# Kernel optimization log

Measured on AMD Instinct MI355X. Metric: run time of the kernel, lower is better.

Reference implementation:

```python
import jax, jax.numpy as jnp
import numpy as np

EMBED_DIM = 1024
NUM_HEADS = 16
HEAD_DIM = EMBED_DIM // NUM_HEADS  # 64
MLP_DIM = 4096
EPS = 1e-5  # torch LayerNorm default


def layer_norm(x, gamma, beta):
    mu = jnp.mean(x, axis=-1, keepdims=True)
    var = jnp.mean(jnp.square(x - mu), axis=-1, keepdims=True)
    return (x - mu) * jax.lax.rsqrt(var + EPS) * gamma + beta


def setup_inputs() -> dict:
    key = jax.random.key(0)
    ks = jax.random.split(key, 12)
    s = 0.02
    x = jax.random.normal(ks[0], (2, 2048, EMBED_DIM), dtype=jnp.float32)
    # per-head qkv projections (Linear(embed_dim, 3*head_dim, bias=False)), stacked over heads
    w_qkv = s * jax.random.normal(ks[1], (NUM_HEADS, EMBED_DIM, 3 * HEAD_DIM), dtype=jnp.float32)
    # per-head output proj (Linear(head_dim, head_dim), with bias)
    w_hproj = s * jax.random.normal(ks[2], (NUM_HEADS, HEAD_DIM, HEAD_DIM), dtype=jnp.float32)
    b_hproj = jnp.zeros((NUM_HEADS, HEAD_DIM), dtype=jnp.float32)
    # MHA final proj (Linear(num_heads*head_dim, embed_dim))
    w_out = s * jax.random.normal(ks[3], (NUM_HEADS * HEAD_DIM, EMBED_DIM), dtype=jnp.float32)
    b_out = jnp.zeros((EMBED_DIM,), dtype=jnp.float32)
    # MLP
    w_fc1 = s * jax.random.normal(ks[4], (EMBED_DIM, MLP_DIM), dtype=jnp.float32)
    b_fc1 = jnp.zeros((MLP_DIM,), dtype=jnp.float32)
    w_fc2 = s * jax.random.normal(ks[5], (MLP_DIM, EMBED_DIM), dtype=jnp.float32)
    b_fc2 = jnp.zeros((EMBED_DIM,), dtype=jnp.float32)
    # layer norms
    g1 = jnp.ones((EMBED_DIM,), dtype=jnp.float32)
    be1 = jnp.zeros((EMBED_DIM,), dtype=jnp.float32)
    g2 = jnp.ones((EMBED_DIM,), dtype=jnp.float32)
    be2 = jnp.zeros((EMBED_DIM,), dtype=jnp.float32)
    return dict(x=x, w_qkv=w_qkv, w_hproj=w_hproj, b_hproj=b_hproj,
                w_out=w_out, b_out=b_out, w_fc1=w_fc1, b_fc1=b_fc1,
                w_fc2=w_fc2, b_fc2=b_fc2, g1=g1, be1=be1, g2=g2, be2=be2)


def reference(x, w_qkv, w_hproj, b_hproj, w_out, b_out,
              w_fc1, b_fc1, w_fc2, b_fc2, g1, be1, g2, be2):
    B, S, D = x.shape
    scale = HEAD_DIM ** (-0.5)

    # ---- MSA branch (pre-norm, dropouts are identity at eval) ----
    xn = layer_norm(x, g1, be1)
    qkv = jnp.einsum('bsd,hdf->bhsf', xn, w_qkv)  # [B,H,S,3*hd]
    q, k, v = jnp.split(qkv, 3, axis=-1)           # each [B,H,S,hd]
    attn = jax.nn.softmax(jnp.einsum('bhsd,bhtd->bhst', q, k) * scale, axis=-1)
    o = jnp.einsum('bhst,bhtd->bhsd', attn, v)     # [B,H,S,hd]
    o = jnp.einsum('bhsd,hde->bhse', o, w_hproj) + b_hproj[None, :, None, :]
    # concat heads along last dim (head 0 first), then final proj
    o = o.transpose(0, 2, 1, 3).reshape(B, S, NUM_HEADS * HEAD_DIM)
    o = o @ w_out + b_out
    x = x + o

    # ---- MLP branch ----
    xn = layer_norm(x, g2, be2)
    h = jax.nn.gelu(xn @ w_fc1 + b_fc1, approximate=False)
    x = x + (h @ w_fc2 + b_fc2)
    return x
```

## Files before the change

kernel.cpp:

```cpp
#include <hip/hip_runtime.h>
#include <hip/hip_bf16.h>
#include <math.h>

#define DEV __device__ __forceinline__

typedef float f32x4 __attribute__((ext_vector_type(4)));
typedef short bf16x8 __attribute__((ext_vector_type(8)));

DEV unsigned short f2bf(float f) {
  union { float f; unsigned int u; } c; c.f = f;
  return (unsigned short)((c.u + 0x7FFF + ((c.u >> 16) & 1)) >> 16);
}
DEV float bf2f(unsigned short u) {
  union { unsigned int u; float f; } c; c.u = ((unsigned int)u) << 16;
  return c.f;
}

#define ASYNC_LD16(gp, lp)                                                     \
  __builtin_amdgcn_global_load_lds(                                            \
      (const __attribute__((address_space(1))) void*)(gp),                     \
      (__attribute__((address_space(3))) void*)(lp), 16, 0, 0)

__global__ void trans_f32_bf16(const float* __restrict__ in, unsigned short* __restrict__ out,
                               int R, int C, long inBatch, long outBatch) {
  __shared__ float tile[64][65];
  int ct = blockIdx.x, rt = blockIdx.y, z = blockIdx.z;
  const float* src = in + (long)z * inBatch + (long)rt * 64 * C + ct * 64;
  unsigned short* dst = out + (long)z * outBatch + (long)ct * 64 * R + rt * 64;
  int t = threadIdx.x, c = t & 63, r0 = t >> 6;
#pragma unroll
  for (int i = 0; i < 16; i++) {
    int r = i * 4 + r0;
    tile[r][c] = src[(long)r * C + c];
  }
  __syncthreads();
#pragma unroll
  for (int i = 0; i < 16; i++) {
    int r = i * 4 + r0;
    dst[(long)r * R + c] = f2bf(tile[c][r]);
  }
}

__global__ void combine_wout(const float* __restrict__ w_hproj, const float* __restrict__ w_out,
                             unsigned short* __restrict__ wcombt) {
  int hd = blockIdx.x;
  int h = hd >> 6, d = hd & 63;
  for (int i = 0; i < 4; i++) {
    int e = threadIdx.x + i * 256;
    float acc = 0.f;
    for (int dp = 0; dp < 64; dp++)
      acc += w_hproj[(h * 64 + d) * 64 + dp] * w_out[(h * 64 + dp) * 1024 + e];
    wcombt[(long)e * 1024 + hd] = f2bf(acc);
  }
}

__global__ void combine_bias(const float* __restrict__ b_hproj, const float* __restrict__ w_out,
                             const float* __restrict__ b_out, float* __restrict__ bcomb) {
  __shared__ float part[8][32];
  int e = blockIdx.x * 32 + (threadIdx.x & 31);
  int ks = threadIdx.x >> 5;
  float acc = 0.f;
  for (int k = ks * 128; k < ks * 128 + 128; k++) acc += b_hproj[k] * w_out[(long)k * 1024 + e];
  part[ks][threadIdx.x & 31] = acc;
  __syncthreads();
  if (threadIdx.x < 32) {
    float s = b_out[e];
#pragma unroll
    for (int i = 0; i < 8; i++) s += part[i][threadIdx.x];
    bcomb[e] = s;
  }
}

__global__ void transpose_v(const unsigned short* __restrict__ in, unsigned short* __restrict__ out) {
  __shared__ unsigned short tile[64][65];
  int st = blockIdx.x, bh = blockIdx.y;
  const unsigned short* src = in + (long)bh * 131072 + (long)st * 64 * 64;
  unsigned short* dst = out + (long)bh * 131072 + (long)st * 64;
  int t = threadIdx.x, c = t & 63, r0 = t >> 6;
#pragma unroll
  for (int i = 0; i < 16; i++) tile[i * 4 + r0][c] = src[(i * 4 + r0) * 64 + c];
  __syncthreads();
  int kb = c >> 4, g = kb >> 1, sub = kb & 1, hi2 = (c >> 2) & 3, jj = c & 3;
  int pos = g * 32 + hi2 * 8 + sub * 4 + jj;
#pragma unroll
  for (int i = 0; i < 16; i++) {
    int d = i * 4 + r0;
    dst[(long)d * 2048 + pos] = tile[c][d];
  }
}

__launch_bounds__(256)
__global__ void ln_kernel(const float* __restrict__ x, const float* __restrict__ g,
                          const float* __restrict__ b, unsigned short* __restrict__ out) {
  int row = blockIdx.x, t = threadIdx.x;
  float4 v = ((const float4*)(x + (long)row * 1024))[t];
  float s = v.x + v.y + v.z + v.w;
  float s2 = v.x * v.x + v.y * v.y + v.z * v.z + v.w * v.w;
  for (int o = 32; o; o >>= 1) { s += __shfl_down(s, o); s2 += __shfl_down(s2, o); }
  __shared__ float red[8];
  int w = t >> 6, l = t & 63;
  if (l == 0) { red[w] = s; red[w + 4] = s2; }
  __syncthreads();
  s = red[0] + red[1] + red[2] + red[3];
  s2 = red[4] + red[5] + red[6] + red[7];
  float mu = s * (1.f / 1024.f);
  float var = s2 * (1.f / 1024.f) - mu * mu;
  float rs = rsqrtf(var + 1e-5f);
  float4 gv = ((const float4*)g)[t];
  float4 bv = ((const float4*)b)[t];
  ushort4 o4;
  o4.x = f2bf((v.x - mu) * rs * gv.x + bv.x);
  o4.y = f2bf((v.y - mu) * rs * gv.y + bv.y);
  o4.z = f2bf((v.z - mu) * rs * gv.z + bv.z);
  o4.w = f2bf((v.w - mu) * rs * gv.w + bv.w);
  ((ushort4*)(out + (long)row * 1024))[t] = o4;
}

template <int ACCUM>
__launch_bounds__(256)
__global__ void reduce_add(const unsigned short* __restrict__ p0,
                           const unsigned short* __restrict__ p1,
                           const float* __restrict__ bias, const float* __restrict__ resid,
                           float* __restrict__ out) {
  int i = blockIdx.x * 256 + threadIdx.x;
  float4 b = ((const float4*)bias)[i & 255];
  float4 r = ACCUM ? ((const float4*)out)[i] : ((const float4*)resid)[i];
  ushort4 a0 = ((const ushort4*)p0)[i];
  ushort4 a1 = ((const ushort4*)p1)[i];
  float4 o;
  o.x = r.x + b.x + bf2f(a0.x) + bf2f(a1.x);
  o.y = r.y + b.y + bf2f(a0.y) + bf2f(a1.y);
  o.z = r.z + b.z + bf2f(a0.z) + bf2f(a1.z);
  o.w = r.w + b.w + bf2f(a0.w) + bf2f(a1.w);
  ((float4*)out)[i] = o;
}

#define EPI_QKV 0
#define EPI_GELU 2
#define EPI_PARTIAL 3

template <int EPI>
__launch_bounds__(512, 2)
__global__ void gemm_p(const unsigned short* __restrict__ A, const unsigned short* __restrict__ Bt,
                       int N, int K, const float* __restrict__ bias,
                       unsigned short* __restrict__ outb,
                       unsigned short* __restrict__ qb, unsigned short* __restrict__ kb,
                       unsigned short* __restrict__ vb,
                       unsigned short* __restrict__ pp0, unsigned short* __restrict__ pp1) {
  __shared__ alignas(16) unsigned short lds_a[3][128 * 64];
  __shared__ alignas(16) unsigned short lds_b[3][256 * 64];
  int gx = gridDim.x, nwg = gx * gridDim.y;
  int orig = blockIdx.y * gx + blockIdx.x;
  int cpx = nwg >> 3;
  int wg = (orig & 7) * cpx + (orig >> 3);
  int bm = wg % gx, bn = wg / gx;

  int tt = K >> 6, Z = gridDim.z, z = blockIdx.z;
  int bq = tt / Z, rem = tt - bq * Z;
  int nk = bq + (z < rem ? 1 : 0);
  int kt0 = z * bq + (z < rem ? z : rem);

  int t = threadIdx.x, w = t >> 6, l = t & 63;
  int wm = w >> 2, wn = w & 3;
  int lr = l & 15, hi = l >> 4;

  f32x4 acc[4][4];
  const f32x4 z4 = {0.f, 0.f, 0.f, 0.f};
#pragma unroll
  for (int m = 0; m < 4; m++)
#pragma unroll
    for (int n = 0; n < 4; n++) acc[m][n] = z4;

#define GSTAGE(buf, kt)                                                        \
  do {                                                                         \
    _Pragma("unroll")                                                          \
    for (int i = 0; i < 2; i++) {                                              \
      int ch = i * 512 + t;                                                    \
      int row = ch >> 3, cs = ch & 7;                                          \
      int csz = cs ^ (row & 7);                                                \
      ASYNC_LD16(A + (long)(bm * 128 + row) * K + (kt0 + (kt)) * 64 + csz * 8, \
                 lds_a[buf] + (size_t)ch * 8);                                 \
    }                                                                          \
    _Pragma("unroll")                                                          \
    for (int i = 0; i < 4; i++) {                                              \
      int ch = i * 512 + t;                                                    \
      int row = ch >> 3, cs = ch & 7;                                          \
      int csz = cs ^ (row & 7);                                                \
      ASYNC_LD16(Bt + (long)(bn * 256 + row) * K + (kt0 + (kt)) * 64 + csz * 8,\
                 lds_b[buf] + (size_t)ch * 8);                                 \
    }                                                                          \
  } while (0)

  GSTAGE(0, 0);
  GSTAGE(1, 1);
  asm volatile("s_waitcnt vmcnt(6)" ::: "memory");
  asm volatile("s_barrier" ::: "memory");

  for (int kt = 0; kt < nk; ++kt) {
    int cur = kt % 3;
    if (kt + 2 < nk) GSTAGE((kt + 2) % 3, kt + 2);
#pragma unroll
    for (int kc = 0; kc < 2; kc++) {
      bf16x8 af[4], bfr[4];
#pragma unroll
      for (int m = 0; m < 4; m++) {
        int row = wm * 64 + m * 16 + lr;
        af[m] = *(const bf16x8*)((const char*)lds_a[cur] + row * 128 +
                                 ((((kc << 2) | hi) ^ (row & 7)) << 4));
      }
#pragma unroll
      for (int n = 0; n < 4; n++) {
        int row = wn * 64 + n * 16 + lr;
        bfr[n] = *(const bf16x8*)((const char*)lds_b[cur] + row * 128 +
                                  ((((kc << 2) | hi) ^ (row & 7)) << 4));
      }
      __builtin_amdgcn_s_setprio(1);
#pragma unroll
      for (int m = 0; m < 4; m++)
#pragma unroll
        for (int n = 0; n < 4; n++)
          acc[m][n] = __builtin_amdgcn_mfma_f32_16x16x32_bf16(af[m], bfr[n], acc[m][n], 0, 0, 0);
      __builtin_amdgcn_s_setprio(0);
    }
    if (kt + 1 < nk) {
      if (kt + 2 < nk) {
        asm volatile("s_waitcnt vmcnt(6)" ::: "memory");
      } else {
        asm volatile("s_waitcnt vmcnt(0)" ::: "memory");
      }
      asm volatile("s_barrier" ::: "memory");
    }
  }
#undef GSTAGE

#pragma unroll
  for (int m = 0; m < 4; m++) {
#pragma unroll
    for (int n = 0; n < 4; n++) {
      int c = bn * 256 + wn * 64 + n * 16 + lr;
#pragma unroll
      for (int j = 0; j < 4; j++) {
        int r = bm * 128 + wm * 64 + m * 16 + hi * 4 + j;
        float val = acc[m][n][j];
        if (EPI == EPI_QKV) {
          int h = c / 192, f = c - h * 192;
          int part = f >> 6, d = f & 63;
          int b = r >> 11, s = r & 2047;
          long idx = ((long)(b * 16 + h) * 2048 + s) * 64 + d;
          if (part == 0) qb[idx] = f2bf(val * 0.18033688011112042f);
          else if (part == 1) kb[idx] = f2bf(val);
          else vb[idx] = f2bf(val);
        } else if (EPI == EPI_GELU) {
          float u = val + bias[c];
          float z2 = u * (0.7978845608f + 0.0356774081f * u * u) * 2.885390082f;
          float e2 = exp2f(z2);
          float th = 1.f - 2.f / (e2 + 1.f);
          outb[(long)r * N + c] = f2bf(0.5f * u * (1.f + th));
        } else {
          unsigned short* pd = (z == 0) ? pp0 : pp1;
          pd[(long)r * N + c] = f2bf(val);
        }
      }
    }
  }
}

__launch_bounds__(256)
__global__ void attn_kernel(const unsigned short* __restrict__ Qg,
                            const unsigned short* __restrict__ Kg,
                            const unsigned short* __restrict__ Vt,
                            unsigned short* __restrict__ Og) {
  __shared__ alignas(16) unsigned short k_lds[2][64 * 64];
  __shared__ alignas(16) unsigned short v_lds[2][64 * 64];
  int orig = blockIdx.y * 32 + blockIdx.x;
  int wg = (orig & 7) * 128 + (orig >> 3);
  int qt = wg & 31, bh = wg >> 5;

  int t = threadIdx.x, w = t >> 6, l = t & 63, lr = l & 15, hi = l >> 4;
  const unsigned short* Qh = Qg + (long)bh * 131072;
  const char* Kh = (const char*)(Kg + (long)bh * 131072);
  const char* Vh = (const char*)(Vt + (long)bh * 131072);

  int qrow = qt * 64 + w * 16 + lr;
  bf16x8 qf0 = *(const bf16x8*)(Qh + (long)qrow * 64 + hi * 8);
  bf16x8 qf1 = *(const bf16x8*)(Qh + (long)qrow * 64 + 32 + hi * 8);
  asm volatile("" :: "v"(qf0), "v"(qf1));

  const f32x4 z4 = {0.f, 0.f, 0.f, 0.f};
  f32x4 accO[4];
#pragma unroll
  for (int j = 0; j < 4; j++) accO[j] = z4;
  float m_q = -1e30f, lsum = 0.f;

#define STAGE(b, kt)                                                           \
  do {                                                                         \
    _Pragma("unroll")                                                          \
    for (int i = 0; i < 2; i++) {                                              \
      int o = (t + i * 256) * 16;                                              \
      int row = o >> 7;                                                        \
      int colb = (o & 127) ^ ((row & 7) << 4);                                 \
      ASYNC_LD16(Kh + (long)((kt) * 64 + row) * 128 + colb,                    \
                 (char*)k_lds[b] + (w * 64 + i * 256) * 16);                   \
      ASYNC_LD16(Vh + (long)row * 4096 + (kt) * 128 + colb,                    \
                 (char*)v_lds[b] + (w * 64 + i * 256) * 16);                   \
    }                                                                          \
  } while (0)

  STAGE(0, 0);

  for (int kt = 0; kt < 32; ++kt) {
    int cur = kt & 1;
    if (kt < 31) {
      STAGE(cur ^ 1, kt + 1);
      asm volatile("s_waitcnt vmcnt(4)" ::: "memory");
    } else {
      asm volatile("s_waitcnt vmcnt(0)" ::: "memory");
    }
    __builtin_amdgcn_s_barrier();

    f32x4 sacc[4];
#pragma unroll
    for (int kbk = 0; kbk < 4; kbk++) sacc[kbk] = z4;
    __builtin_amdgcn_s_setprio(1);
#pragma unroll
    for (int kbk = 0; kbk < 4; kbk++) {
      int krow = kbk * 16 + lr;
      int sw = (krow & 7) << 4;
      const char* kbase = (const char*)k_lds[cur] + krow * 128;
      bf16x8 kf0 = *(const bf16x8*)(kbase + ((hi * 16) ^ sw));
      bf16x8 kf1 = *(const bf16x8*)(kbase + ((64 + hi * 16) ^ sw));
      sacc[kbk] = __builtin_amdgcn_mfma_f32_16x16x32_bf16(kf0, qf0, sacc[kbk], 0, 0, 0);
      sacc[kbk] = __builtin_amdgcn_mfma_f32_16x16x32_bf16(kf1, qf1, sacc[kbk], 0, 0, 0);
    }
    __builtin_amdgcn_s_setprio(0);

    float mx = -1e30f;
#pragma unroll
    for (int kbk = 0; kbk < 4; kbk++)
#pragma unroll
      for (int r = 0; r < 4; r++) mx = fmaxf(mx, sacc[kbk][r]);
    mx = fmaxf(mx, __shfl_xor(mx, 16));
    mx = fmaxf(mx, __shfl_xor(mx, 32));
    if (!__all(mx <= m_q + 8.f)) {
      float mnew = fmaxf(m_q, mx);
      float fac = exp2f(m_q - mnew);
      m_q = mnew;
      lsum *= fac;
      float fj[4];
#pragma unroll
      for (int j = 0; j < 4; j++) fj[j] = __shfl(fac, ((l >> 4) << 2) | j);
#pragma unroll
      for (int db = 0; db < 4; db++)
#pragma unroll
        for (int j = 0; j < 4; j++) accO[db][j] *= fj[j];
    }
    float rs = 0.f;
#pragma unroll
    for (int kbk = 0; kbk < 4; kbk++)
#pragma unroll
      for (int r = 0; r < 4; r++) {
        float p = exp2f(sacc[kbk][r] - m_q);
        sacc[kbk][r] = p;
        rs += p;
      }
    rs += __shfl_xor(rs, 16);
    rs += __shfl_xor(rs, 32);
    lsum += rs;

    bf16x8 pa0, pa1;
#pragma unroll
    for (int r = 0; r < 4; r++) {
      pa0[r] = (short)f2bf(sacc[0][r]);
      pa0[r + 4] = (short)f2bf(sacc[1][r]);
      pa1[r] = (short)f2bf(sacc[2][r]);
      pa1[r + 4] = (short)f2bf(sacc[3][r]);
    }

    __builtin_amdgcn_s_setprio(1);
#pragma unroll
    for (int g = 0; g < 2; g++) {
      bf16x8 pf = g ? pa1 : pa0;
#pragma unroll
      for (int db = 0; db < 4; db++) {
        int d = db * 16 + lr;
        int sw = (d & 7) << 4;
        bf16x8 vf = *(const bf16x8*)((const char*)v_lds[cur] + d * 128 + ((g * 64 + hi * 16) ^ sw));
        accO[db] = __builtin_amdgcn_mfma_f32_16x16x32_bf16(pf, vf, accO[db], 0, 0, 0);
      }
    }
    __builtin_amdgcn_s_setprio(0);

    if (kt < 31) {
      asm volatile("s_waitcnt lgkmcnt(0)" ::: "memory");
      __builtin_amdgcn_s_barrier();
    }
  }
#undef STAGE

  float linv[4];
#pragma unroll
  for (int j = 0; j < 4; j++) linv[j] = 1.f / __shfl(lsum, ((l >> 4) << 2) | j);

  int b = bh >> 4, h = bh & 15;
#pragma unroll
  for (int db = 0; db < 4; db++)
#pragma unroll
    for (int j = 0; j < 4; j++) {
      int s = qt * 64 + w * 16 + hi * 4 + j;
      Og[((long)(b * 2048 + s)) * 1024 + h * 64 + db * 16 + lr] = f2bf(accO[db][j] * linv[j]);
    }
}

extern "C" void kernel_launch(void* const* d_in, const int* in_sizes, int n_in,
                              void* d_out, int out_size, void* d_ws, size_t ws_size,
                              hipStream_t stream) {
  const float* x = (const float*)d_in[0];
  const float* w_qkv = (const float*)d_in[1];
  const float* w_hproj = (const float*)d_in[2];
  const float* b_hproj = (const float*)d_in[3];
  const float* w_out = (const float*)d_in[4];
  const float* b_out = (const float*)d_in[5];
  const float* w_fc1 = (const float*)d_in[6];
  const float* b_fc1 = (const float*)d_in[7];
  const float* w_fc2 = (const float*)d_in[8];
  const float* b_fc2 = (const float*)d_in[9];
  const float* g1 = (const float*)d_in[10];
  const float* be1 = (const float*)d_in[11];
  const float* g2 = (const float*)d_in[12];
  const float* be2 = (const float*)d_in[13];
  float* out = (float*)d_out;

  char* ws = (char*)d_ws;
  unsigned short* wqkvt = (unsigned short*)(ws + 0);
  unsigned short* wfc1t = (unsigned short*)(ws + 6291456);
  unsigned short* wfc2t = (unsigned short*)(ws + 14680064);
  unsigned short* wcombt = (unsigned short*)(ws + 23068672);
  float* bcomb = (float*)(ws + 25165824);
  unsigned short* xn = (unsigned short*)(ws + 25169920);
  unsigned short* qb = (unsigned short*)(ws + 33558528);
  unsigned short* kb = (unsigned short*)(ws + 41947136);
  unsigned short* vb = (unsigned short*)(ws + 50335744);
  unsigned short* attn_o = (unsigned short*)(ws + 58724352);
  unsigned short* h1 = qb;
  unsigned short* vt = xn;
  unsigned short* f2p0 = wfc1t;
  unsigned short* f2p1 = xn;

  trans_f32_bf16<<<dim3(3, 16, 16), 256, 0, stream>>>(w_qkv, wqkvt, 1024, 192,
                                                      196608L, 196608L);
  trans_f32_bf16<<<dim3(64, 16, 1), 256, 0, stream>>>(w_fc1, wfc1t, 1024, 4096, 0, 0);
  trans_f32_bf16<<<dim3(16, 64, 1), 256, 0, stream>>>(w_fc2, wfc2t, 4096, 1024, 0, 0);
  combine_wout<<<1024, 256, 0, stream>>>(w_hproj, w_out, wcombt);
  combine_bias<<<32, 256, 0, stream>>>(b_hproj, w_out, b_out, bcomb);

  ln_kernel<<<4096, 256, 0, stream>>>(x, g1, be1, xn);
  gemm_p<EPI_QKV><<<dim3(32, 12, 1), 512, 0, stream>>>(xn, wqkvt, 3072, 1024,
      nullptr, nullptr, qb, kb, vb, nullptr, nullptr);
  transpose_v<<<dim3(32, 32), 256, 0, stream>>>(vb, vt);
  attn_kernel<<<dim3(32, 32), 256, 0, stream>>>(qb, kb, vt, attn_o);
  gemm_p<EPI_PARTIAL><<<dim3(32, 4, 2), 512, 0, stream>>>(attn_o, wcombt, 1024, 1024,
      nullptr, nullptr, nullptr, nullptr, nullptr, qb, kb);
  reduce_add<0><<<4096, 256, 0, stream>>>(qb, kb, bcomb, x, out);

  ln_kernel<<<4096, 256, 0, stream>>>(out, g2, be2, xn);
  gemm_p<EPI_GELU><<<dim3(32, 16, 1), 512, 0, stream>>>(xn, wfc1t, 4096, 1024,
      b_fc1, h1, nullptr, nullptr, nullptr, nullptr, nullptr);
  gemm_p<EPI_PARTIAL><<<dim3(32, 4, 2), 512, 0, stream>>>(h1, wfc2t, 1024, 4096,
      nullptr, nullptr, nullptr, nullptr, nullptr, f2p0, f2p1);
  reduce_add<1><<<4096, 256, 0, stream>>>(f2p0, f2p1, b_fc2, nullptr, out);
}
```

Baseline: 346.5 us.

## Restructure GEMM into 8-phase double-buffered schedule with 256-row tiles for QKV/FC1

Replaces the triple-buffered GEMM main loop with a double-buffered loop split into four barrier-separated compute phases. The next tile's global-to-LDS loads are interleaved between those phases, so memory traffic overlaps the MFMA work at a finer grain. The tile height becomes a template parameter: the QKV and FC1 GEMMs now use 256x256 tiles, halving the grid in M and increasing operand reuse, while the output-projection and FC2 GEMMs keep 128-row tiles. This adds barriers per iteration, and the 256-row variant needs more registers and a larger LDS footprint, with fewer blocks available to fill the GPU.

```diff
diff --git a/kernel.cpp b/kernel.cpp
--- a/kernel.cpp
+++ b/kernel.cpp
@@ -139,16 +139,20 @@
 #define EPI_GELU 2
 #define EPI_PARTIAL 3
 
-template <int EPI>
+template <int EPI, int BM>
 __launch_bounds__(512, 2)
-__global__ void gemm_p(const unsigned short* __restrict__ A, const unsigned short* __restrict__ Bt,
+__global__ void gemm8p(const unsigned short* __restrict__ A, const unsigned short* __restrict__ Bt,
                        int N, int K, const float* __restrict__ bias,
                        unsigned short* __restrict__ outb,
                        unsigned short* __restrict__ qb, unsigned short* __restrict__ kb,
                        unsigned short* __restrict__ vb,
                        unsigned short* __restrict__ pp0, unsigned short* __restrict__ pp1) {
-  __shared__ alignas(16) unsigned short lds_a[3][128 * 64];
-  __shared__ alignas(16) unsigned short lds_b[3][256 * 64];
+  constexpr int MF = BM / 32;
+  constexpr int MH = MF / 2;
+  constexpr int WM = BM / 2;
+  __shared__ alignas(16) unsigned short lds_a[2][BM * 64];
+  __shared__ alignas(16) unsigned short lds_b[2][256 * 64];
+
   int gx = gridDim.x, nwg = gx * gridDim.y;
   int orig = blockIdx.y * gx + blockIdx.x;
   int cpx = nwg >> 3;
@@ -164,83 +168,92 @@
   int wm = w >> 2, wn = w & 3;
   int lr = l & 15, hi = l >> 4;
 
-  f32x4 acc[4][4];
+  f32x4 acc[MF][4];
   const f32x4 z4 = {0.f, 0.f, 0.f, 0.f};
 #pragma unroll
-  for (int m = 0; m < 4; m++)
+  for (int m = 0; m < MF; m++)
 #pragma unroll
     for (int n = 0; n < 4; n++) acc[m][n] = z4;
 
-#define GSTAGE(buf, kt)                                                        \
-  do {                                                                         \
-    _Pragma("unroll")                                                          \
-    for (int i = 0; i < 2; i++) {                                              \
-      int ch = i * 512 + t;                                                    \
-      int row = ch >> 3, cs = ch & 7;                                          \
-      int csz = cs ^ (row & 7);                                                \
-      ASYNC_LD16(A + (long)(bm * 128 + row) * K + (kt0 + (kt)) * 64 + csz * 8, \
-                 lds_a[buf] + (size_t)ch * 8);                                 \
+#define STAGE_A(buf, kt, s)                                                    \
+  { int row_ = (s) * 64 + (t >> 3), csz_ = (t & 7) ^ (row_ & 7);               \
+    ASYNC_LD16(A + (long)(bm * BM + row_) * K + (kt0 + (kt)) * 64 + csz_ * 8,  \
+               lds_a[buf] + (size_t)((s) * 512 + t) * 8); }
+#define STAGE_B(buf, kt, s)                                                    \
+  { int row_ = (s) * 64 + (t >> 3), csz_ = (t & 7) ^ (row_ & 7);               \
+    ASYNC_LD16(Bt + (long)(bn * 256 + row_) * K + (kt0 + (kt)) * 64 + csz_ * 8,\
+               lds_b[buf] + (size_t)((s) * 512 + t) * 8); }
+
+#define PHASE(cur, kc, mh)                                                     \
+  {                                                                            \
+    bf16x8 af4[MH], bf4[4];                                                    \
+    _Pragma("unroll") for (int m4 = 0; m4 < MH; m4++) {                        \
+      int row_ = wm * WM + (mh) * (WM / 2) + m4 * 16 + lr;                     \
+      af4[m4] = *(const bf16x8*)((const char*)lds_a[cur] + row_ * 128 +        \
+                                 ((((kc)*4 + hi) ^ (row_ & 7)) << 4));         \
     }                                                                          \
-    _Pragma("unroll")                                                          \
-    for (int i = 0; i < 4; i++) {                                              \
-      int ch = i * 512 + t;                                                    \
-      int row = ch >> 3, cs = ch & 7;                                          \
-      int csz = cs ^ (row & 7);                                                \
-      ASYNC_LD16(Bt + (long)(bn * 256 + row) * K + (kt0 + (kt)) * 64 + csz * 8,\
-                 lds_b[buf] + (size_t)ch * 8);                                 \
+    _Pragma("unroll") for (int n = 0; n < 4; n++) {                            \
+      int row_ = wn * 64 + n * 16 + lr;                                        \
+      bf4[n] = *(const bf16x8*)((const char*)lds_b[cur] + row_ * 128 +         \
+                                ((((kc)*4 + hi) ^ (row_ & 7)) << 4));          \
     }                                                                          \
-  } while (0)
-
-  GSTAGE(0, 0);
-  GSTAGE(1, 1);
-  asm volatile("s_waitcnt vmcnt(6)" ::: "memory");
-  asm volatile("s_barrier" ::: "memory");
-
-  for (int kt = 0; kt < nk; ++kt) {
-    int cur = kt % 3;
-    if (kt + 2 < nk) GSTAGE((kt + 2) % 3, kt + 2);
-#pragma unroll
-    for (int kc = 0; kc < 2; kc++) {
-      bf16x8 af[4], bfr[4];
-#pragma unroll
-      for (int m = 0; m < 4; m++) {
-        int row = wm * 64 + m * 16 + lr;
-        af[m] = *(const bf16x8*)((const char*)lds_a[cur] + row * 128 +
-                                 ((((kc << 2) | hi) ^ (row & 7)) << 4));
-      }
-#pragma unroll
-      for (int n = 0; n < 4; n++) {
-        int row = wn * 64 + n * 16 + lr;
-        bfr[n] = *(const bf16x8*)((const char*)lds_b[cur] + row * 128 +
-                                  ((((kc << 2) | hi) ^ (row & 7)) << 4));
-      }
-      __builtin_amdgcn_s_setprio(1);
-#pragma unroll
-      for (int m = 0; m < 4; m++)
-#pragma unroll
-        for (int n = 0; n < 4; n++)
-          acc[m][n] = __builtin_amdgcn_mfma_f32_16x16x32_bf16(af[m], bfr[n], acc[m][n], 0, 0, 0);
-      __builtin_amdgcn_s_setprio(0);
-    }
-    if (kt + 1 < nk) {
-      if (kt + 2 < nk) {
-        asm volatile("s_waitcnt vmcnt(6)" ::: "memory");
-      } else {
-        asm volatile("s_waitcnt vmcnt(0)" ::: "memory");
-      }
-      asm volatile("s_barrier" ::: "memory");
-    }
-  }
-#undef GSTAGE
-
-#pragma unroll
-  for (int m = 0; m < 4; m++) {
+    __builtin_amdgcn_s_barrier();                                              \
+    __builtin_amdgcn_s_setprio(1);                                             \
+    _Pragma("unroll") for (int m4 = 0; m4 < MH; m4++)                          \
+      _Pragma("unroll") for (int n = 0; n < 4; n++)                            \
+        acc[(mh) * MH + m4][n] = __builtin_amdgcn_mfma_f32_16x16x32_bf16(      \
+            af4[m4], bf4[n], acc[(mh) * MH + m4][n], 0, 0, 0);                 \
+    __builtin_amdgcn_s_setprio(0);                                             \
+  }
+
+  if (BM == 256) {
+    STAGE_A(0, 0, 0); STAGE_A(0, 0, 1); STAGE_A(0, 0, 2); STAGE_A(0, 0, 3);
+    STAGE_B(0, 0, 0); STAGE_B(0, 0, 1); STAGE_B(0, 0, 2); STAGE_B(0, 0, 3);
+    STAGE_A(1, 1, 0); STAGE_A(1, 1, 2);
+    asm volatile("s_waitcnt vmcnt(2)" ::: "memory");
+  } else {
+    STAGE_A(0, 0, 0); STAGE_A(0, 0, 1);
+    STAGE_B(0, 0, 0); STAGE_B(0, 0, 1); STAGE_B(0, 0, 2); STAGE_B(0, 0, 3);
+    asm volatile("s_waitcnt vmcnt(0)" ::: "memory");
+  }
+  __builtin_amdgcn_s_barrier();
+
+  for (int T = 0; T < nk; ++T) {
+    int cur = T & 1, nxt = cur ^ 1;
+    bool s1 = (T + 1 < nk), s2 = (T + 2 < nk);
+    if (s1) {
+      if (BM == 256) { STAGE_A(nxt, T + 1, 1); STAGE_A(nxt, T + 1, 3); }
+      else           { STAGE_A(nxt, T + 1, 0); STAGE_A(nxt, T + 1, 1); }
+    }
+    PHASE(cur, 0, 0);
+    __builtin_amdgcn_s_barrier();
+    if (s1) { STAGE_B(nxt, T + 1, 0); STAGE_B(nxt, T + 1, 1); }
+    PHASE(cur, 0, 1);
+    __builtin_amdgcn_s_barrier();
+    if (s1) { STAGE_B(nxt, T + 1, 2); STAGE_B(nxt, T + 1, 3); }
+    PHASE(cur, 1, 0);
+    __builtin_amdgcn_s_barrier();
+    if (BM == 256 && s2) { STAGE_A(cur, T + 2, 0); STAGE_A(cur, T + 2, 2); }
+    PHASE(cur, 1, 1);
+    if (BM == 256 && s2) {
+      asm volatile("s_waitcnt vmcnt(2)" ::: "memory");
+    } else {
+      asm volatile("s_waitcnt vmcnt(0)" ::: "memory");
+    }
+    __builtin_amdgcn_s_barrier();
+  }
+#undef STAGE_A
+#undef STAGE_B
+#undef PHASE
+
+#pragma unroll
+  for (int m = 0; m < MF; m++) {
 #pragma unroll
     for (int n = 0; n < 4; n++) {
       int c = bn * 256 + wn * 64 + n * 16 + lr;
 #pragma unroll
       for (int j = 0; j < 4; j++) {
-        int r = bm * 128 + wm * 64 + m * 16 + hi * 4 + j;
+        int r = bm * BM + wm * WM + m * 16 + hi * 4 + j;
         float val = acc[m][n][j];
         if (EPI == EPI_QKV) {
           int h = c / 192, f = c - h * 192;
@@ -454,18 +467,18 @@
   combine_bias<<<32, 256, 0, stream>>>(b_hproj, w_out, b_out, bcomb);
 
   ln_kernel<<<4096, 256, 0, stream>>>(x, g1, be1, xn);
-  gemm_p<EPI_QKV><<<dim3(32, 12, 1), 512, 0, stream>>>(xn, wqkvt, 3072, 1024,
+  gemm8p<EPI_QKV, 256><<<dim3(16, 12, 1), 512, 0, stream>>>(xn, wqkvt, 3072, 1024,
       nullptr, nullptr, qb, kb, vb, nullptr, nullptr);
   transpose_v<<<dim3(32, 32), 256, 0, stream>>>(vb, vt);
   attn_kernel<<<dim3(32, 32), 256, 0, stream>>>(qb, kb, vt, attn_o);
-  gemm_p<EPI_PARTIAL><<<dim3(32, 4, 2), 512, 0, stream>>>(attn_o, wcombt, 1024, 1024,
+  gemm8p<EPI_PARTIAL, 128><<<dim3(32, 4, 2), 512, 0, stream>>>(attn_o, wcombt, 1024, 1024,
       nullptr, nullptr, nullptr, nullptr, nullptr, qb, kb);
   reduce_add<0><<<4096, 256, 0, stream>>>(qb, kb, bcomb, x, out);
 
   ln_kernel<<<4096, 256, 0, stream>>>(out, g2, be2, xn);
-  gemm_p<EPI_GELU><<<dim3(32, 16, 1), 512, 0, stream>>>(xn, wfc1t, 4096, 1024,
+  gemm8p<EPI_GELU, 256><<<dim3(16, 16, 1), 512, 0, stream>>>(xn, wfc1t, 4096, 1024,
       b_fc1, h1, nullptr, nullptr, nullptr, nullptr, nullptr);
-  gemm_p<EPI_PARTIAL><<<dim3(32, 4, 2), 512, 0, stream>>>(h1, wfc2t, 1024, 4096,
+  gemm8p<EPI_PARTIAL, 128><<<dim3(32, 4, 2), 512, 0, stream>>>(h1, wfc2t, 1024, 4096,
       nullptr, nullptr, nullptr, nullptr, nullptr, f2p0, f2p1);
   reduce_add<1><<<4096, 256, 0, stream>>>(f2p0, f2p1, b_fc2, nullptr, out);
 }
```

Result: slower. 374.7 us, median of 3 (+8.2%).

## Replace triple-buffered 128x256 GEMM with single-buffer 128x128 tile kernel

Applied to the files above, without the earlier changes.

The GEMM kernel moves from a 512-thread, 128x256 tile with a three-stage async LDS pipeline to a 256-thread, 128x128 tile with one LDS buffer. Each k-step now loads, waits on vmcnt(0), synchronises and computes. Grids double along N to keep coverage. The smaller LDS footprint and block size aim for more resident workgroups and more blocks per GPU, at the cost of losing load/compute overlap inside a block and reusing each tile less.

```diff
diff --git a/kernel.cpp b/kernel.cpp
--- a/kernel.cpp
+++ b/kernel.cpp
@@ -140,15 +140,15 @@
 #define EPI_PARTIAL 3
 
 template <int EPI>
-__launch_bounds__(512, 2)
-__global__ void gemm_p(const unsigned short* __restrict__ A, const unsigned short* __restrict__ Bt,
+__launch_bounds__(256, 3)
+__global__ void gemm97(const unsigned short* __restrict__ A, const unsigned short* __restrict__ Bt,
                        int N, int K, const float* __restrict__ bias,
                        unsigned short* __restrict__ outb,
                        unsigned short* __restrict__ qb, unsigned short* __restrict__ kb,
                        unsigned short* __restrict__ vb,
                        unsigned short* __restrict__ pp0, unsigned short* __restrict__ pp1) {
-  __shared__ alignas(16) unsigned short lds_a[3][128 * 64];
-  __shared__ alignas(16) unsigned short lds_b[3][256 * 64];
+  __shared__ alignas(16) unsigned short lds_a[128 * 64];
+  __shared__ alignas(16) unsigned short lds_b[128 * 64];
   int gx = gridDim.x, nwg = gx * gridDim.y;
   int orig = blockIdx.y * gx + blockIdx.x;
   int cpx = nwg >> 3;
@@ -161,7 +161,7 @@
   int kt0 = z * bq + (z < rem ? z : rem);
 
   int t = threadIdx.x, w = t >> 6, l = t & 63;
-  int wm = w >> 2, wn = w & 3;
+  int wm = w >> 1, wn = w & 1;
   int lr = l & 15, hi = l >> 4;
 
   f32x4 acc[4][4];
@@ -171,47 +171,37 @@
 #pragma unroll
     for (int n = 0; n < 4; n++) acc[m][n] = z4;
 
-#define GSTAGE(buf, kt)                                                        \
-  do {                                                                         \
-    _Pragma("unroll")                                                          \
-    for (int i = 0; i < 2; i++) {                                              \
-      int ch = i * 512 + t;                                                    \
-      int row = ch >> 3, cs = ch & 7;                                          \
-      int csz = cs ^ (row & 7);                                                \
-      ASYNC_LD16(A + (long)(bm * 128 + row) * K + (kt0 + (kt)) * 64 + csz * 8, \
-                 lds_a[buf] + (size_t)ch * 8);                                 \
-    }                                                                          \
-    _Pragma("unroll")                                                          \
-    for (int i = 0; i < 4; i++) {                                              \
-      int ch = i * 512 + t;                                                    \
-      int row = ch >> 3, cs = ch & 7;                                          \
-      int csz = cs ^ (row & 7);                                                \
-      ASYNC_LD16(Bt + (long)(bn * 256 + row) * K + (kt0 + (kt)) * 64 + csz * 8,\
-                 lds_b[buf] + (size_t)ch * 8);                                 \
-    }                                                                          \
-  } while (0)
-
-  GSTAGE(0, 0);
-  GSTAGE(1, 1);
-  asm volatile("s_waitcnt vmcnt(6)" ::: "memory");
-  asm volatile("s_barrier" ::: "memory");
-
   for (int kt = 0; kt < nk; ++kt) {
-    int cur = kt % 3;
-    if (kt + 2 < nk) GSTAGE((kt + 2) % 3, kt + 2);
+    __syncthreads();
+#pragma unroll
+    for (int i = 0; i < 4; i++) {
+      int ch = i * 256 + t;
+      int row = ch >> 3, csz = (ch & 7) ^ (row & 7);
+      ASYNC_LD16(A + (long)(bm * 128 + row) * K + (kt0 + kt) * 64 + csz * 8,
+                 lds_a + (size_t)ch * 8);
+    }
+#pragma unroll
+    for (int i = 0; i < 4; i++) {
+      int ch = i * 256 + t;
+      int row = ch >> 3, csz = (ch & 7) ^ (row & 7);
+      ASYNC_LD16(Bt + (long)(bn * 128 + row) * K + (kt0 + kt) * 64 + csz * 8,
+                 lds_b + (size_t)ch * 8);
+    }
+    asm volatile("s_waitcnt vmcnt(0)" ::: "memory");
+    __builtin_amdgcn_s_barrier();
 #pragma unroll
     for (int kc = 0; kc < 2; kc++) {
       bf16x8 af[4], bfr[4];
 #pragma unroll
       for (int m = 0; m < 4; m++) {
         int row = wm * 64 + m * 16 + lr;
-        af[m] = *(const bf16x8*)((const char*)lds_a[cur] + row * 128 +
+        af[m] = *(const bf16x8*)((const char*)lds_a + row * 128 +
                                  ((((kc << 2) | hi) ^ (row & 7)) << 4));
       }
 #pragma unroll
       for (int n = 0; n < 4; n++) {
         int row = wn * 64 + n * 16 + lr;
-        bfr[n] = *(const bf16x8*)((const char*)lds_b[cur] + row * 128 +
+        bfr[n] = *(const bf16x8*)((const char*)lds_b + row * 128 +
                                   ((((kc << 2) | hi) ^ (row & 7)) << 4));
       }
       __builtin_amdgcn_s_setprio(1);
@@ -222,22 +212,13 @@
           acc[m][n] = __builtin_amdgcn_mfma_f32_16x16x32_bf16(af[m], bfr[n], acc[m][n], 0, 0, 0);
       __builtin_amdgcn_s_setprio(0);
     }
-    if (kt + 1 < nk) {
-      if (kt + 2 < nk) {
-        asm volatile("s_waitcnt vmcnt(6)" ::: "memory");
-      } else {
-        asm volatile("s_waitcnt vmcnt(0)" ::: "memory");
-      }
-      asm volatile("s_barrier" ::: "memory");
-    }
-  }
-#undef GSTAGE
+  }
 
 #pragma unroll
   for (int m = 0; m < 4; m++) {
 #pragma unroll
     for (int n = 0; n < 4; n++) {
-      int c = bn * 256 + wn * 64 + n * 16 + lr;
+      int c = bn * 128 + wn * 64 + n * 16 + lr;
 #pragma unroll
       for (int j = 0; j < 4; j++) {
         int r = bm * 128 + wm * 64 + m * 16 + hi * 4 + j;
@@ -454,18 +435,18 @@
   combine_bias<<<32, 256, 0, stream>>>(b_hproj, w_out, b_out, bcomb);
 
   ln_kernel<<<4096, 256, 0, stream>>>(x, g1, be1, xn);
-  gemm_p<EPI_QKV><<<dim3(32, 12, 1), 512, 0, stream>>>(xn, wqkvt, 3072, 1024,
+  gemm97<EPI_QKV><<<dim3(32, 24, 1), 256, 0, stream>>>(xn, wqkvt, 3072, 1024,
       nullptr, nullptr, qb, kb, vb, nullptr, nullptr);
   transpose_v<<<dim3(32, 32), 256, 0, stream>>>(vb, vt);
   attn_kernel<<<dim3(32, 32), 256, 0, stream>>>(qb, kb, vt, attn_o);
-  gemm_p<EPI_PARTIAL><<<dim3(32, 4, 2), 512, 0, stream>>>(attn_o, wcombt, 1024, 1024,
+  gemm97<EPI_PARTIAL><<<dim3(32, 8, 2), 256, 0, stream>>>(attn_o, wcombt, 1024, 1024,
       nullptr, nullptr, nullptr, nullptr, nullptr, qb, kb);
   reduce_add<0><<<4096, 256, 0, stream>>>(qb, kb, bcomb, x, out);
 
   ln_kernel<<<4096, 256, 0, stream>>>(out, g2, be2, xn);
-  gemm_p<EPI_GELU><<<dim3(32, 16, 1), 512, 0, stream>>>(xn, wfc1t, 4096, 1024,
+  gemm97<EPI_GELU><<<dim3(32, 32, 1), 256, 0, stream>>>(xn, wfc1t, 4096, 1024,
       b_fc1, h1, nullptr, nullptr, nullptr, nullptr, nullptr);
-  gemm_p<EPI_PARTIAL><<<dim3(32, 4, 2), 512, 0, stream>>>(h1, wfc2t, 1024, 4096,
+  gemm97<EPI_PARTIAL><<<dim3(32, 8, 2), 256, 0, stream>>>(h1, wfc2t, 1024, 4096,
       nullptr, nullptr, nullptr, nullptr, nullptr, f2p0, f2p1);
   reduce_add<1><<<4096, 256, 0, stream>>>(f2p0, f2p1, b_fc2, nullptr, out);
 }
```

New measurement: 308.7 us, median of 2. -10.9%, faster.
